# Kernel optimization log

Hardware: AMD Instinct MI355X
Metric: run time of the kernel (lower is better)

## Reference

```python
import jax, jax.numpy as jnp
import numpy as np

B, D, S, H = 16384, 512, 3, 8
HD = D // H


def setup_inputs() -> dict:
    key = jax.random.key(0)
    ks = jax.random.split(key, 12)
    n = lambda k, shp, s=0.02: jax.random.normal(k, shp, jnp.float32) * s
    return {
        'x': jax.random.normal(ks[0], (B, D), jnp.float32),
        'h_prev': jax.random.normal(ks[1], (S, B, D), jnp.float32),
        'c_prev': jax.random.normal(ks[2], (S, B, D), jnp.float32),
        'ssm_state': jax.random.normal(ks[3], (B, D), jnp.float32),
        'Wt': n(ks[4], (S, D, D)),          # per-scale transform Linear weight
        'bt': jnp.zeros((S, D), jnp.float32),
        'ln_g': jnp.ones((S, D), jnp.float32),
        'ln_b': jnp.zeros((S, D), jnp.float32),
        'W_ih': n(ks[5], (S, 4 * D, D)),    # LSTMCell input weights (i,f,g,o)
        'W_hh': n(ks[6], (S, 4 * D, D)),
        'b_ih': jnp.zeros((S, 4 * D), jnp.float32),
        'b_hh': jnp.zeros((S, 4 * D), jnp.float32),
        'decays': jnp.linspace(0.5, 0.9, S, dtype=jnp.float32),
        'in_proj_w': n(ks[7], (3 * D, D)),  # MHA packed q/k/v projections
        'in_proj_b': jnp.zeros((3 * D,), jnp.float32),
        'out_proj_w': n(ks[8], (D, D)),
        'out_proj_b': jnp.zeros((D,), jnp.float32),
        'mix_w': n(ks[9], (D, S * D)),
        'mix_b': jnp.zeros((D,), jnp.float32),
    }


def reference(x, h_prev, c_prev, ssm_state, Wt, bt, ln_g, ln_b,
              W_ih, W_hh, b_ih, b_hh, decays,
              in_proj_w, in_proj_b, out_proj_w, out_proj_b, mix_w, mix_b):
    # per-scale transform: Linear -> LayerNorm -> exact GELU  (S,B,D)
    xs = jnp.einsum('bd,sed->sbe', x, Wt) + bt[:, None, :]
    mu = xs.mean(-1, keepdims=True)
    var = ((xs - mu) ** 2).mean(-1, keepdims=True)
    xs = (xs - mu) * jax.lax.rsqrt(var + 1e-5) * ln_g[:, None, :] + ln_b[:, None, :]
    xs = jax.nn.gelu(xs, approximate=False)
    # LSTMCell (all scales vectorized); gate order i,f,g,o as in torch
    gates = (jnp.einsum('sbe,sge->sbg', xs, W_ih) + b_ih[:, None, :]
             + jnp.einsum('sbd,sgd->sbg', h_prev, W_hh) + b_hh[:, None, :])
    ig, fg, gg, og = jnp.split(gates, 4, axis=-1)
    c_lstm = jax.nn.sigmoid(fg) * c_prev + jax.nn.sigmoid(ig) * jnp.tanh(gg)
    h_new = jax.nn.sigmoid(og) * jnp.tanh(c_lstm)
    d = decays[:, None, None]
    c_new = d * c_prev + (1.0 - d) * c_lstm  # decay blend (h uses pre-blend c)
    # torch.cat(outputs, dim=-1): scale-major feature blocks  (B, S*D)
    multi = jnp.transpose(h_new, (1, 0, 2)).reshape(B, S * D)
    # MHA fusion: query = ssm_state (1 token), keys/values = scale outputs
    Wq, Wk, Wv = jnp.split(in_proj_w, 3, axis=0)
    bq, bk, bv = jnp.split(in_proj_b, 3)
    q = (ssm_state @ Wq.T + bq).reshape(B, H, HD)
    k = (jnp.einsum('sbd,ed->sbe', h_new, Wk) + bk).reshape(S, B, H, HD)
    v = (jnp.einsum('sbd,ed->sbe', h_new, Wv) + bv).reshape(S, B, H, HD)
    scale = jnp.float32(1.0 / np.sqrt(HD))
    attn = jax.nn.softmax(jnp.einsum('bhd,sbhd->bhs', q, k) * scale, axis=-1)
    fused = jnp.einsum('bhs,sbhd->bhd', attn, v).reshape(B, D) @ out_proj_w.T + out_proj_b
    out = multi @ mix_w.T + mix_b + fused
    return out, h_new, c_new
```

## Files before the change

### kernel.cpp

```cpp
#include <hip/hip_runtime.h>
#include <stdint.h>


#define Bq 16384
#define Dq 512
#define Sq 3
#define Hq 8

typedef unsigned short u16;
typedef __bf16 bf16x8 __attribute__((ext_vector_type(8)));
typedef float f32x4 __attribute__((ext_vector_type(4)));
typedef u16 u16x8 __attribute__((ext_vector_type(8)));
typedef u16 u16x4v __attribute__((ext_vector_type(4)));

__device__ __forceinline__ u16 f2bf(float f) {
    union { float f; uint32_t u; } c; c.f = f;
    uint32_t u = c.u;
    return (u16)((u + 0x7fffu + ((u >> 16) & 1u)) >> 16);
}
__device__ __forceinline__ float bf2f(u16 h) {
    union { uint32_t u; float f; } c; c.u = ((uint32_t)h) << 16;
    return c.f;
}

__device__ __forceinline__ void async16(const u16* g, u16* l) {
    __builtin_amdgcn_global_load_lds(
        (__attribute__((address_space(1))) void*)const_cast<u16*>(g),
        (__attribute__((address_space(3))) void*)l, 16, 0, 0);
}

struct CvtArgs {
    const float* src[9];
    u16* dst[9];
    long long bound[9];
};

__global__ __launch_bounds__(256) void cvt_all_kernel(CvtArgs a, long long total)
{
    long long i = ((long long)blockIdx.x * 256 + threadIdx.x) * 4;
    if (i >= total) return;
    const float* s = a.src[0];
    u16* d = a.dst[0];
    long long base = 0;
#pragma unroll
    for (int t = 0; t < 8; ++t) {
        if (i >= a.bound[t]) { s = a.src[t + 1]; d = a.dst[t + 1]; base = a.bound[t]; }
    }
    const long long l = i - base;
    float4 v = *(const float4*)(s + l);
    u16x4v o; o[0] = f2bf(v.x); o[1] = f2bf(v.y); o[2] = f2bf(v.z); o[3] = f2bf(v.w);
    *(u16x4v*)(d + l) = o;
}

struct SegR { const u16* A; int lda; const u16* W; int ldw; };
struct Seg  { const u16* A; long long Az; int lda; const u16* W; long long Wz; int ldw; };

template<int NSEG, int OUTBF>
__device__ __forceinline__ void gemm_core(const SegR* segs,
                                          const float* __restrict__ bias0,
                                          const float* __restrict__ bias1,
                                          void* __restrict__ outp, int ldo)
{
    __shared__ u16 As[128 * 64];
    __shared__ u16 Bs[128 * 64];
    const int tid  = threadIdx.x;
    const int lane = tid & 63;
    const int wv   = tid >> 6;
    const int wm   = wv >> 1, wn = wv & 1;
    const long long rowBase = (long long)blockIdx.y * 128;
    const long long colBase = (long long)blockIdx.x * 128;

    f32x4 acc[4][4];
#pragma unroll
    for (int a = 0; a < 4; ++a)
#pragma unroll
        for (int b = 0; b < 4; ++b) acc[a][b] = (f32x4){0.f, 0.f, 0.f, 0.f};

    const int srow  = tid >> 3;
    const int swcol = (((tid & 7) ^ (srow & 7)) << 3);
    const int dcol  = (tid & 7) << 3;
    const int lrow  = lane & 15;
    const int lquad = lane >> 4;

#pragma unroll
    for (int sg = 0; sg < NSEG; ++sg) {
        const int lda = segs[sg].lda, ldw = segs[sg].ldw;
        const u16* Ab = segs[sg].A + (rowBase + srow) * (long long)lda + swcol;
        const u16* Wb = segs[sg].W + (colBase + srow) * (long long)ldw + swcol;
        for (int kt = 0; kt < 512; kt += 64) {
#pragma unroll
            for (int i = 0; i < 4; ++i) {
                async16(Ab + (long long)(i * 32) * lda + kt, &As[(i * 32 + srow) * 64 + dcol]);
                async16(Wb + (long long)(i * 32) * ldw + kt, &Bs[(i * 32 + srow) * 64 + dcol]);
            }
            __syncthreads();
#pragma unroll
            for (int kk = 0; kk < 64; kk += 32) {
                const int ca = ((((kk >> 3) + lquad) ^ (lrow & 7)) << 3);
                bf16x8 af[4], bw[4];
#pragma unroll
                for (int t = 0; t < 4; ++t)
                    af[t] = *(const bf16x8*)&As[(wm * 64 + t * 16 + lrow) * 64 + ca];
#pragma unroll
                for (int t = 0; t < 4; ++t)
                    bw[t] = *(const bf16x8*)&Bs[(wn * 64 + t * 16 + lrow) * 64 + ca];
#pragma unroll
                for (int mt = 0; mt < 4; ++mt)
#pragma unroll
                    for (int nt = 0; nt < 4; ++nt)
                        acc[mt][nt] = __builtin_amdgcn_mfma_f32_16x16x32_bf16(
                            af[mt], bw[nt], acc[mt][nt], 0, 0, 0);
            }
            __syncthreads();
        }
    }

#pragma unroll
    for (int nt = 0; nt < 4; ++nt) {
        const long long col = colBase + wn * 64 + nt * 16 + lrow;
        float bvv = bias0[col];
        if (bias1) bvv += bias1[col];
#pragma unroll
        for (int mt = 0; mt < 4; ++mt) {
            const long long row0 = rowBase + wm * 64 + mt * 16 + lquad * 4;
#pragma unroll
            for (int r = 0; r < 4; ++r) {
                const float val = acc[mt][nt][r] + bvv;
                const long long o = (row0 + r) * (long long)ldo + col;
                if (OUTBF) ((u16*)outp)[o] = f2bf(val);
                else       ((float*)outp)[o] = val;
            }
        }
    }
}

template<int NSEG, int OUTBF>
__global__ __launch_bounds__(256, 2)
void gemm_seg_kernel(Seg s0, Seg s1, Seg s2, Seg s3,
                     const float* bias0, long long b0z,
                     const float* bias1, long long b1z,
                     void* outp, long long outz, int ldo)
{
    const int z = blockIdx.z;
    const Seg segsIn[4] = {s0, s1, s2, s3};
    SegR segs[NSEG];
#pragma unroll
    for (int i = 0; i < NSEG; ++i) {
        segs[i].A   = segsIn[i].A + (long long)z * segsIn[i].Az;
        segs[i].lda = segsIn[i].lda;
        segs[i].W   = segsIn[i].W + (long long)z * segsIn[i].Wz;
        segs[i].ldw = segsIn[i].ldw;
    }
    gemm_core<NSEG, OUTBF>(segs,
        bias0 + (long long)z * b0z,
        bias1 ? bias1 + (long long)z * b1z : nullptr,
        OUTBF ? (void*)((u16*)outp + (long long)z * outz)
              : (void*)((float*)outp + (long long)z * outz),
        ldo);
}

__global__ __launch_bounds__(256, 2)
void qkv_gemm_kernel(const u16* __restrict__ hnew, const u16* __restrict__ ssm,
                     const u16* __restrict__ inpj, const float* __restrict__ ipb,
                     u16* __restrict__ kout, u16* __restrict__ vout,
                     u16* __restrict__ qout)
{
    const int z = blockIdx.z;
    const long long BD = (long long)Bq * Dq;
    SegR seg[1];
    const float* bias;
    u16* out;
    if (z < 3) {
        seg[0].A = hnew + z * BD;        seg[0].W = inpj + Dq * Dq;
        bias = ipb + Dq;                 out = kout + z * BD;
    } else if (z < 6) {
        seg[0].A = hnew + (z - 3) * BD;  seg[0].W = inpj + 2 * Dq * Dq;
        bias = ipb + 2 * Dq;             out = vout + (z - 3) * BD;
    } else {
        seg[0].A = ssm;                  seg[0].W = inpj;
        bias = ipb;                      out = qout;
    }
    seg[0].lda = Dq; seg[0].ldw = Dq;
    gemm_core<1, 1>(seg, bias, nullptr, out, Dq);
}

__global__ __launch_bounds__(256) void ln_gelu_kernel(u16* __restrict__ xs,
                                                      const float* __restrict__ ln_g,
                                                      const float* __restrict__ ln_b)
{
    const int lane = threadIdx.x & 63;
    const int wvi  = threadIdx.x >> 6;
    const long long row = (long long)blockIdx.x * 4 + wvi;
    const int s = (int)(row >> 14);
    u16* p = xs + row * Dq + lane * 8;
    u16x8 u = *(const u16x8*)p;
    float v[8];
    float sum = 0.f, sq = 0.f;
#pragma unroll
    for (int j = 0; j < 8; ++j) { v[j] = bf2f(u[j]); sum += v[j]; sq += v[j] * v[j]; }
#pragma unroll
    for (int m = 32; m >= 1; m >>= 1) { sum += __shfl_xor(sum, m, 64); sq += __shfl_xor(sq, m, 64); }
    const float mu   = sum * (1.f / 512.f);
    const float var  = sq * (1.f / 512.f) - mu * mu;
    const float rstd = rsqrtf(var + 1e-5f);
    const float* g = ln_g + (size_t)s * Dq + lane * 8;
    const float* b = ln_b + (size_t)s * Dq + lane * 8;
    u16x8 o;
#pragma unroll
    for (int j = 0; j < 8; ++j) {
        float y  = (v[j] - mu) * rstd * g[j] + b[j];
        float ge = 0.5f * y * (1.f + erff(y * 0.70710678118654752f));
        o[j] = f2bf(ge);
    }
    *(u16x8*)p = o;
}

__global__ __launch_bounds__(256) void lstm_kernel(const u16* __restrict__ gates_all,
                                                   const float* __restrict__ cprev,
                                                   const float* __restrict__ decays,
                                                   float* __restrict__ hout,
                                                   float* __restrict__ cout,
                                                   u16* __restrict__ hbf)
{
    const long long i = ((long long)blockIdx.x * 256 + threadIdx.x) * 4;
    const int s = (int)(i >> 23);
    const long long off = i & ((1LL << 23) - 1);
    const long long bi = off >> 9;
    const int d = (int)(off & 511);
    const u16* g = gates_all + ((long long)s << 25) + bi * 2048 + d;
    u16x4v ig = *(const u16x4v*)(g);
    u16x4v fg = *(const u16x4v*)(g + 512);
    u16x4v gg = *(const u16x4v*)(g + 1024);
    u16x4v og = *(const u16x4v*)(g + 1536);
    float4 cp4 = *(const float4*)(cprev + i);
    float cpa[4] = {cp4.x, cp4.y, cp4.z, cp4.w};
    const float dec = decays[s];
    float hv[4], cv[4]; u16x4v hb;
#pragma unroll
    for (int j = 0; j < 4; ++j) {
        float igf = 1.f / (1.f + expf(-bf2f(ig[j])));
        float fgf = 1.f / (1.f + expf(-bf2f(fg[j])));
        float ggf = tanhf(bf2f(gg[j]));
        float ogf = 1.f / (1.f + expf(-bf2f(og[j])));
        float cl  = fgf * cpa[j] + igf * ggf;
        float hn  = ogf * tanhf(cl);
        hv[j] = hn;
        cv[j] = dec * cpa[j] + (1.f - dec) * cl;
        hb[j] = f2bf(hn);
    }
    *(float4*)(hout + i) = make_float4(hv[0], hv[1], hv[2], hv[3]);
    *(float4*)(cout + i) = make_float4(cv[0], cv[1], cv[2], cv[3]);
    *(u16x4v*)(hbf + i)  = hb;
}

__global__ __launch_bounds__(256) void attn_kernel(const u16* __restrict__ q,
                                                   const u16* __restrict__ k,
                                                   const u16* __restrict__ v,
                                                   u16* __restrict__ fused)
{
    const int lane = threadIdx.x & 63;
    const int wvi  = threadIdx.x >> 6;
    const long long idx = (long long)blockIdx.x * 4 + wvi;
    const long long off = idx * 64 + lane;
    const float qv = bf2f(q[off]);
    float sc[3];
#pragma unroll
    for (int s = 0; s < 3; ++s) {
        float p = qv * bf2f(k[(long long)s * Bq * Dq + off]);
#pragma unroll
        for (int m = 32; m >= 1; m >>= 1) p += __shfl_xor(p, m, 64);
        sc[s] = p * 0.125f;
    }
    const float mx = fmaxf(sc[0], fmaxf(sc[1], sc[2]));
    const float e0 = expf(sc[0] - mx), e1 = expf(sc[1] - mx), e2 = expf(sc[2] - mx);
    const float inv = 1.f / (e0 + e1 + e2);
    const float f = (e0 * bf2f(v[off]) +
                     e1 * bf2f(v[(long long)Bq * Dq + off]) +
                     e2 * bf2f(v[2LL * Bq * Dq + off])) * inv;
    fused[off] = f2bf(f);
}

extern "C" void kernel_launch(void* const* d_in, const int* in_sizes, int n_in,
                              void* d_out, int out_size, void* d_ws, size_t ws_size,
                              hipStream_t stream)
{
    (void)in_sizes; (void)n_in; (void)out_size; (void)ws_size;

    const float* x         = (const float*)d_in[0];
    const float* h_prev    = (const float*)d_in[1];
    const float* c_prev    = (const float*)d_in[2];
    const float* ssm       = (const float*)d_in[3];
    const float* Wt        = (const float*)d_in[4];
    const float* bt        = (const float*)d_in[5];
    const float* ln_g      = (const float*)d_in[6];
    const float* ln_b      = (const float*)d_in[7];
    const float* W_ih      = (const float*)d_in[8];
    const float* W_hh      = (const float*)d_in[9];
    const float* b_ih      = (const float*)d_in[10];
    const float* b_hh      = (const float*)d_in[11];
    const float* decays    = (const float*)d_in[12];
    const float* in_proj_w = (const float*)d_in[13];
    const float* in_proj_b = (const float*)d_in[14];
    const float* out_proj_w= (const float*)d_in[15];
    const float* out_proj_b= (const float*)d_in[16];
    const float* mix_w     = (const float*)d_in[17];
    const float* mix_b     = (const float*)d_in[18];
    float* out = (float*)d_out;

    const long long BD = (long long)Bq * Dq;

    u16* base = (u16*)d_ws;
    size_t off = 0;
    auto walloc = [&](size_t n) { u16* p = base + off; off += (n + 4095) & ~(size_t)4095; return p; };
    u16* wt_bf    = walloc((size_t)Sq * Dq * Dq);
    u16* wih_bf   = walloc((size_t)Sq * 4 * Dq * Dq);
    u16* whh_bf   = walloc((size_t)Sq * 4 * Dq * Dq);
    u16* inpj_bf  = walloc((size_t)3 * Dq * Dq);
    u16* outpj_bf = walloc((size_t)Dq * Dq);
    u16* mix_bf   = walloc((size_t)Dq * Sq * Dq);
    u16* x_bf     = walloc((size_t)Bq * Dq);
    u16* ssm_bf   = walloc((size_t)Bq * Dq);
    u16* hprev_bf = walloc((size_t)Sq * Bq * Dq);
    u16* xs_bf    = walloc((size_t)Sq * Bq * Dq);
    u16* gates_bf = walloc((size_t)Sq * Bq * 4 * Dq);
    u16* hnew_bf  = walloc((size_t)Sq * Bq * Dq);
    u16* k_bf  = xs_bf;
    u16* v_bf  = hprev_bf;
    u16* q_bf  = gates_bf;
    u16* fu_bf = gates_bf + BD;

    {
        CvtArgs a;
        const float* srcs[9] = {x, ssm, h_prev, Wt, W_ih, W_hh, in_proj_w, out_proj_w, mix_w};
        u16* dsts[9] = {x_bf, ssm_bf, hprev_bf, wt_bf, wih_bf, whh_bf, inpj_bf, outpj_bf, mix_bf};
        const long long ns[9] = {BD, BD, Sq * BD,
                                 (long long)Sq * Dq * Dq, (long long)Sq * 4 * Dq * Dq,
                                 (long long)Sq * 4 * Dq * Dq, (long long)3 * Dq * Dq,
                                 (long long)Dq * Dq, (long long)Dq * Sq * Dq};
        long long acc = 0;
        for (int i = 0; i < 9; ++i) { a.src[i] = srcs[i]; a.dst[i] = dsts[i]; acc += ns[i]; a.bound[i] = acc; }
        cvt_all_kernel<<<dim3((unsigned)((acc / 4 + 255) / 256)), 256, 0, stream>>>(a, acc);
    }

    Seg zs{nullptr, 0, 0, nullptr, 0, 0};

    {
        Seg a{x_bf, 0, Dq, wt_bf, (long long)Dq * Dq, Dq};
        gemm_seg_kernel<1, 1><<<dim3(Dq / 128, Bq / 128, Sq), 256, 0, stream>>>(
            a, zs, zs, zs, bt, Dq, nullptr, 0, xs_bf, BD, Dq);
    }
    ln_gelu_kernel<<<dim3(Sq * Bq / 4), 256, 0, stream>>>(xs_bf, ln_g, ln_b);

    {
        Seg a{xs_bf, BD, Dq, wih_bf, (long long)4 * Dq * Dq, Dq};
        Seg b{hprev_bf, BD, Dq, whh_bf, (long long)4 * Dq * Dq, Dq};
        gemm_seg_kernel<2, 1><<<dim3(4 * Dq / 128, Bq / 128, Sq), 256, 0, stream>>>(
            a, b, zs, zs, b_ih, 4 * Dq, b_hh, 4 * Dq, gates_bf, 4 * BD, 4 * Dq);
    }
    lstm_kernel<<<dim3(Sq * Bq * Dq / 1024), 256, 0, stream>>>(
        gates_bf, c_prev, decays,
        out + BD,
        out + 4 * BD,
        hnew_bf);

    qkv_gemm_kernel<<<dim3(Dq / 128, Bq / 128, 7), 256, 0, stream>>>(
        hnew_bf, ssm_bf, inpj_bf, in_proj_b, k_bf, v_bf, q_bf);

    attn_kernel<<<dim3(Bq * Hq / 4), 256, 0, stream>>>(q_bf, k_bf, v_bf, fu_bf);

    {
        Seg a0{hnew_bf, 0, Dq, mix_bf, 0, Sq * Dq};
        Seg a1{hnew_bf + BD, 0, Dq, mix_bf + Dq, 0, Sq * Dq};
        Seg a2{hnew_bf + 2 * BD, 0, Dq, mix_bf + 2 * Dq, 0, Sq * Dq};
        Seg a3{fu_bf, 0, Dq, outpj_bf, 0, Dq};
        gemm_seg_kernel<4, 0><<<dim3(Dq / 128, Bq / 128, 1), 256, 0, stream>>>(
            a0, a1, a2, a3, mix_b, 0, out_proj_b, 0, out, 0, Dq);
    }
}
```

Measured before the change: 1.018 ms.

## Use 256x256-tile 8-wave GEMM with 4-stage async pipeline; widen elementwise kernels

```diff
diff --git a/kernel.cpp b/kernel.cpp
--- a/kernel.cpp
+++ b/kernel.cpp
@@ -29,6 +29,13 @@
         (__attribute__((address_space(3))) void*)l, 16, 0, 0);
 }
 
+__device__ __forceinline__ float sigf(float x) {
+    return __builtin_amdgcn_rcpf(1.f + __expf(-x));
+}
+__device__ __forceinline__ float tanhfast(float x) {
+    return 1.f - 2.f * __builtin_amdgcn_rcpf(1.f + __expf(2.f * x));
+}
+
 struct CvtArgs {
     const float* src[9];
     u16* dst[9];
@@ -37,7 +44,7 @@
 
 __global__ __launch_bounds__(256) void cvt_all_kernel(CvtArgs a, long long total)
 {
-    long long i = ((long long)blockIdx.x * 256 + threadIdx.x) * 4;
+    long long i = ((long long)blockIdx.x * 256 + threadIdx.x) * 8;
     if (i >= total) return;
     const float* s = a.src[0];
     u16* d = a.dst[0];
@@ -47,9 +54,12 @@
         if (i >= a.bound[t]) { s = a.src[t + 1]; d = a.dst[t + 1]; base = a.bound[t]; }
     }
     const long long l = i - base;
-    float4 v = *(const float4*)(s + l);
-    u16x4v o; o[0] = f2bf(v.x); o[1] = f2bf(v.y); o[2] = f2bf(v.z); o[3] = f2bf(v.w);
-    *(u16x4v*)(d + l) = o;
+    float4 v0 = *(const float4*)(s + l);
+    float4 v1 = *(const float4*)(s + l + 4);
+    u16x8 o;
+    o[0] = f2bf(v0.x); o[1] = f2bf(v0.y); o[2] = f2bf(v0.z); o[3] = f2bf(v0.w);
+    o[4] = f2bf(v1.x); o[5] = f2bf(v1.y); o[6] = f2bf(v1.z); o[7] = f2bf(v1.w);
+    *(u16x8*)(d + l) = o;
 }
 
 struct SegR { const u16* A; int lda; const u16* W; int ldw; };
@@ -159,11 +169,165 @@
         ldo);
 }
 
-__global__ __launch_bounds__(256, 2)
-void qkv_gemm_kernel(const u16* __restrict__ hnew, const u16* __restrict__ ssm,
-                     const u16* __restrict__ inpj, const float* __restrict__ ipb,
-                     u16* __restrict__ kout, u16* __restrict__ vout,
-                     u16* __restrict__ qout)
+template<int NSEG>
+__device__ __forceinline__ void gemm256_core(const SegR* segs,
+                                             const float* __restrict__ bias0,
+                                             const float* __restrict__ bias1,
+                                             u16* __restrict__ outp, int ldo)
+{
+    __shared__ u16 lds[4 * 16384];
+
+    const int tid  = threadIdx.x;
+    const int lane = tid & 63;
+    const int wv   = tid >> 6;
+    const int wm   = wv >> 2;
+    const int wn   = wv & 3;
+
+    const int nx  = gridDim.x;
+    const int nwg = nx * gridDim.y;
+    int lg = blockIdx.y * nx + blockIdx.x;
+    if ((nwg & 7) == 0) {
+        const int cpx = nwg >> 3;
+        lg = (lg & 7) * cpx + (lg >> 3);
+    }
+    const long long rowBase = (long long)(lg / nx) * 256;
+    const long long colBase = (long long)(lg % nx) * 256;
+
+    f32x4 acc[8][4];
+#pragma unroll
+    for (int i = 0; i < 8; ++i)
+#pragma unroll
+        for (int j = 0; j < 4; ++j) acc[i][j] = (f32x4){0.f, 0.f, 0.f, 0.f};
+
+    const u16* pa0[2]; const u16* pa1[2];
+    const u16* pb0[2]; const u16* pb1[2];
+#pragma unroll
+    for (int li = 0; li < 2; ++li) {
+        const int o = li * 512 + tid;
+        const int R = o >> 3;
+        const int c = (o & 7) ^ (R & 7);
+        const int r = 2 * R + (c >> 2);
+        const int k = (c & 3) * 8;
+        pa0[li] = segs[0].A + (rowBase + r) * (long long)segs[0].lda + k;
+        pb0[li] = segs[0].W + (colBase + r) * (long long)segs[0].ldw + k;
+        pa1[li] = pa0[li]; pb1[li] = pb0[li];
+        if (NSEG > 1) {
+            pa1[li] = segs[1].A + (rowBase + r) * (long long)segs[1].lda + k;
+            pb1[li] = segs[1].W + (colBase + r) * (long long)segs[1].ldw + k;
+        }
+    }
+
+    int oa[8];
+#pragma unroll
+    for (int i = 0; i < 8; ++i) {
+        const int r = wm * 128 + i * 16 + (lane & 15);
+        const int R = r >> 1;
+        const int c = (((r & 1) << 2) | (lane >> 4)) ^ (R & 7);
+        oa[i] = (R * 8 + c) * 8;
+    }
+    int ob[4];
+#pragma unroll
+    for (int j = 0; j < 4; ++j) {
+        const int r = wn * 64 + j * 16 + (lane & 15);
+        const int R = r >> 1;
+        const int c = (((r & 1) << 2) | (lane >> 4)) ^ (R & 7);
+        ob[j] = 8192 + (R * 8 + c) * 8;
+    }
+
+    auto stage = [&](int slot, int t) {
+        const long long kt = (long long)(t & 15) * 32;
+        u16* sb = &lds[slot * 16384];
+        const bool s1 = (NSEG > 1) && (t >> 4);
+#pragma unroll
+        for (int li = 0; li < 2; ++li) {
+            const u16* ap = s1 ? pa1[li] : pa0[li];
+            const u16* bp = s1 ? pb1[li] : pb0[li];
+            async16(ap + kt, sb + li * 4096 + tid * 8);
+            async16(bp + kt, sb + 8192 + li * 4096 + tid * 8);
+        }
+    };
+
+    auto compute = [&](int t) {
+        const u16* sb = &lds[(t & 3) * 16384];
+        bf16x8 af[8], bw[4];
+#pragma unroll
+        for (int i = 0; i < 8; ++i) af[i] = *(const bf16x8*)(sb + oa[i]);
+#pragma unroll
+        for (int j = 0; j < 4; ++j) bw[j] = *(const bf16x8*)(sb + ob[j]);
+        __builtin_amdgcn_s_setprio(1);
+#pragma unroll
+        for (int i = 0; i < 8; ++i)
+#pragma unroll
+            for (int j = 0; j < 4; ++j)
+                acc[i][j] = __builtin_amdgcn_mfma_f32_16x16x32_bf16(
+                    af[i], bw[j], acc[i][j], 0, 0, 0);
+        __builtin_amdgcn_s_setprio(0);
+    };
+
+    const int nt = NSEG * 16;
+
+    stage(0, 0);
+    stage(1, 1);
+#pragma unroll 1
+    for (int t = 0; t < nt - 2; ++t) {
+        stage((t + 2) & 3, t + 2);
+        asm volatile("s_waitcnt vmcnt(8)" ::: "memory");
+        __builtin_amdgcn_s_barrier();
+        asm volatile("" ::: "memory");
+        compute(t);
+    }
+    asm volatile("s_waitcnt vmcnt(4)" ::: "memory");
+    __builtin_amdgcn_s_barrier();
+    asm volatile("" ::: "memory");
+    compute(nt - 2);
+    asm volatile("s_waitcnt vmcnt(0)" ::: "memory");
+    __builtin_amdgcn_s_barrier();
+    asm volatile("" ::: "memory");
+    compute(nt - 1);
+
+    const bool hb1 = (bias1 != nullptr);
+#pragma unroll
+    for (int j = 0; j < 4; ++j) {
+        const long long col = colBase + wn * 64 + j * 16 + (lane & 15);
+        float bv = bias0[col];
+        if (hb1) bv += bias1[col];
+#pragma unroll
+        for (int i = 0; i < 8; ++i) {
+            const long long row0 = rowBase + wm * 128 + i * 16 + (lane >> 4) * 4;
+#pragma unroll
+            for (int r = 0; r < 4; ++r)
+                outp[(row0 + r) * (long long)ldo + col] = f2bf(acc[i][j][r] + bv);
+        }
+    }
+}
+
+template<int NSEG>
+__global__ __launch_bounds__(512, 2)
+void gemm256_seg_kernel(Seg s0, Seg s1,
+                        const float* bias0, long long b0z,
+                        const float* bias1, long long b1z,
+                        u16* outp, long long outz, int ldo)
+{
+    const int z = blockIdx.z;
+    SegR segs[2];
+    segs[0].A = s0.A + (long long)z * s0.Az; segs[0].lda = s0.lda;
+    segs[0].W = s0.W + (long long)z * s0.Wz; segs[0].ldw = s0.ldw;
+    segs[1] = segs[0];
+    if (NSEG > 1) {
+        segs[1].A = s1.A + (long long)z * s1.Az; segs[1].lda = s1.lda;
+        segs[1].W = s1.W + (long long)z * s1.Wz; segs[1].ldw = s1.ldw;
+    }
+    gemm256_core<NSEG>(segs,
+        bias0 + (long long)z * b0z,
+        bias1 ? bias1 + (long long)z * b1z : nullptr,
+        outp + (long long)z * outz, ldo);
+}
+
+__global__ __launch_bounds__(512, 2)
+void qkv256_kernel(const u16* __restrict__ hnew, const u16* __restrict__ ssm,
+                   const u16* __restrict__ inpj, const float* __restrict__ ipb,
+                   u16* __restrict__ kout, u16* __restrict__ vout,
+                   u16* __restrict__ qout)
 {
     const int z = blockIdx.z;
     const long long BD = (long long)Bq * Dq;
@@ -181,7 +345,7 @@
         bias = ipb;                      out = qout;
     }
     seg[0].lda = Dq; seg[0].ldw = Dq;
-    gemm_core<1, 1>(seg, bias, nullptr, out, Dq);
+    gemm256_core<1>(seg, bias, nullptr, out, Dq);
 }
 
 __global__ __launch_bounds__(256) void ln_gelu_kernel(u16* __restrict__ xs,
@@ -222,35 +386,38 @@
                                                    float* __restrict__ cout,
                                                    u16* __restrict__ hbf)
 {
-    const long long i = ((long long)blockIdx.x * 256 + threadIdx.x) * 4;
+    const long long i = ((long long)blockIdx.x * 256 + threadIdx.x) * 8;
     const int s = (int)(i >> 23);
     const long long off = i & ((1LL << 23) - 1);
     const long long bi = off >> 9;
     const int d = (int)(off & 511);
     const u16* g = gates_all + ((long long)s << 25) + bi * 2048 + d;
-    u16x4v ig = *(const u16x4v*)(g);
-    u16x4v fg = *(const u16x4v*)(g + 512);
-    u16x4v gg = *(const u16x4v*)(g + 1024);
-    u16x4v og = *(const u16x4v*)(g + 1536);
-    float4 cp4 = *(const float4*)(cprev + i);
-    float cpa[4] = {cp4.x, cp4.y, cp4.z, cp4.w};
+    u16x8 ig = *(const u16x8*)(g);
+    u16x8 fg = *(const u16x8*)(g + 512);
+    u16x8 gg = *(const u16x8*)(g + 1024);
+    u16x8 og = *(const u16x8*)(g + 1536);
+    float4 cp0 = *(const float4*)(cprev + i);
+    float4 cp1 = *(const float4*)(cprev + i + 4);
+    float cpa[8] = {cp0.x, cp0.y, cp0.z, cp0.w, cp1.x, cp1.y, cp1.z, cp1.w};
     const float dec = decays[s];
-    float hv[4], cv[4]; u16x4v hb;
-#pragma unroll
-    for (int j = 0; j < 4; ++j) {
-        float igf = 1.f / (1.f + expf(-bf2f(ig[j])));
-        float fgf = 1.f / (1.f + expf(-bf2f(fg[j])));
-        float ggf = tanhf(bf2f(gg[j]));
-        float ogf = 1.f / (1.f + expf(-bf2f(og[j])));
+    float hv[8], cv[8]; u16x8 hb;
+#pragma unroll
+    for (int j = 0; j < 8; ++j) {
+        float igf = sigf(bf2f(ig[j]));
+        float fgf = sigf(bf2f(fg[j]));
+        float ggf = tanhfast(bf2f(gg[j]));
+        float ogf = sigf(bf2f(og[j]));
         float cl  = fgf * cpa[j] + igf * ggf;
-        float hn  = ogf * tanhf(cl);
+        float hn  = ogf * tanhfast(cl);
         hv[j] = hn;
         cv[j] = dec * cpa[j] + (1.f - dec) * cl;
         hb[j] = f2bf(hn);
     }
-    *(float4*)(hout + i) = make_float4(hv[0], hv[1], hv[2], hv[3]);
-    *(float4*)(cout + i) = make_float4(cv[0], cv[1], cv[2], cv[3]);
-    *(u16x4v*)(hbf + i)  = hb;
+    *(float4*)(hout + i)     = make_float4(hv[0], hv[1], hv[2], hv[3]);
+    *(float4*)(hout + i + 4) = make_float4(hv[4], hv[5], hv[6], hv[7]);
+    *(float4*)(cout + i)     = make_float4(cv[0], cv[1], cv[2], cv[3]);
+    *(float4*)(cout + i + 4) = make_float4(cv[4], cv[5], cv[6], cv[7]);
+    *(u16x8*)(hbf + i)       = hb;
 }
 
 __global__ __launch_bounds__(256) void attn_kernel(const u16* __restrict__ q,
@@ -339,31 +506,31 @@
                                  (long long)Dq * Dq, (long long)Dq * Sq * Dq};
         long long acc = 0;
         for (int i = 0; i < 9; ++i) { a.src[i] = srcs[i]; a.dst[i] = dsts[i]; acc += ns[i]; a.bound[i] = acc; }
-        cvt_all_kernel<<<dim3((unsigned)((acc / 4 + 255) / 256)), 256, 0, stream>>>(a, acc);
+        cvt_all_kernel<<<dim3((unsigned)((acc / 8 + 255) / 256)), 256, 0, stream>>>(a, acc);
     }
 
     Seg zs{nullptr, 0, 0, nullptr, 0, 0};
 
     {
         Seg a{x_bf, 0, Dq, wt_bf, (long long)Dq * Dq, Dq};
-        gemm_seg_kernel<1, 1><<<dim3(Dq / 128, Bq / 128, Sq), 256, 0, stream>>>(
-            a, zs, zs, zs, bt, Dq, nullptr, 0, xs_bf, BD, Dq);
+        gemm256_seg_kernel<1><<<dim3(Dq / 256, Bq / 256, Sq), 512, 0, stream>>>(
+            a, zs, bt, Dq, nullptr, 0, xs_bf, BD, Dq);
     }
     ln_gelu_kernel<<<dim3(Sq * Bq / 4), 256, 0, stream>>>(xs_bf, ln_g, ln_b);
 
     {
         Seg a{xs_bf, BD, Dq, wih_bf, (long long)4 * Dq * Dq, Dq};
         Seg b{hprev_bf, BD, Dq, whh_bf, (long long)4 * Dq * Dq, Dq};
-        gemm_seg_kernel<2, 1><<<dim3(4 * Dq / 128, Bq / 128, Sq), 256, 0, stream>>>(
-            a, b, zs, zs, b_ih, 4 * Dq, b_hh, 4 * Dq, gates_bf, 4 * BD, 4 * Dq);
-    }
-    lstm_kernel<<<dim3(Sq * Bq * Dq / 1024), 256, 0, stream>>>(
+        gemm256_seg_kernel<2><<<dim3(4 * Dq / 256, Bq / 256, Sq), 512, 0, stream>>>(
+            a, b, b_ih, 4 * Dq, b_hh, 4 * Dq, gates_bf, 4 * BD, 4 * Dq);
+    }
+    lstm_kernel<<<dim3((unsigned)(Sq * BD / 2048)), 256, 0, stream>>>(
         gates_bf, c_prev, decays,
         out + BD,
         out + 4 * BD,
         hnew_bf);
 
-    qkv_gemm_kernel<<<dim3(Dq / 128, Bq / 128, 7), 256, 0, stream>>>(
+    qkv256_kernel<<<dim3(Dq / 256, Bq / 256, 7), 512, 0, stream>>>(
         hnew_bf, ssm_bf, inpj_bf, in_proj_b, k_bf, v_bf, q_bf);
 
     attn_kernel<<<dim3(Bq * Hq / 4), 256, 0, stream>>>(q_bf, k_bf, v_bf, fu_bf);
```

After: 1.067 ms. 1.05x slower.
